# Kernel optimization log

Measured on AMD Instinct MI355X. Metric: run time of the kernel, lower is better.

The kernel has to match this reference:

```python
import jax, jax.numpy as jnp
import numpy as np

EPS = 1e-5
NEG = -1000000.0
H = 8

def layer_norm(v, g, b):
    mu = jnp.mean(v, axis=-1, keepdims=True)
    var = jnp.var(v, axis=-1, keepdims=True)
    return (v - mu) * jax.lax.rsqrt(var + EPS) * g + b

def setup_inputs() -> dict:
    key = jax.random.key(0)
    ks = jax.random.split(key, 12)
    B, T, Tc, D, Dc = 8, 2048, 512, 1024, 512
    s = lambda fan: 1.0 / np.sqrt(fan)
    return {
        'query': jax.random.normal(ks[0], (B, T, D), jnp.float32),
        'x': jax.random.normal(ks[1], (B, T, D), jnp.float32),
        'cond_emb': jax.random.normal(ks[2], (B, Tc, Dc), jnp.float32),
        'src_mask': jax.random.uniform(ks[3], (B, T, 1), jnp.float32),
        'cond_mask': jax.random.uniform(ks[4], (B, Tc, 1), jnp.float32),
        'norm_x_g': jnp.ones((D,), jnp.float32),
        'norm_x_b': jnp.zeros((D,), jnp.float32),
        'norm_c_g': jnp.ones((Dc,), jnp.float32),
        'norm_c_b': jnp.zeros((Dc,), jnp.float32),
        'W_kc': jax.random.normal(ks[5], (D, Dc), jnp.float32) * s(Dc),
        'b_kc': jnp.zeros((D,), jnp.float32),
        'W_vc': jax.random.normal(ks[6], (D, Dc), jnp.float32) * s(Dc),
        'b_vc': jnp.zeros((D,), jnp.float32),
        'W_kx': jax.random.normal(ks[7], (D, D), jnp.float32) * s(D),
        'b_kx': jnp.zeros((D,), jnp.float32),
        'W_vx': jax.random.normal(ks[8], (D, D), jnp.float32) * s(D),
        'b_vx': jnp.zeros((D,), jnp.float32),
        'W_y': jax.random.normal(ks[9], (D, D), jnp.float32) * s(D),
        'b_y': jnp.zeros((D,), jnp.float32),
    }

def reference(query, x, cond_emb, src_mask, cond_mask,
              norm_x_g, norm_x_b, norm_c_g, norm_c_b,
              W_kc, b_kc, W_vc, b_vc, W_kx, b_kx, W_vx, b_vx, W_y, b_y):
    B, T, D = x.shape
    Tc = cond_emb.shape[1]
    N = T + Tc
    xn = layer_norm(x, norm_x_g, norm_x_b)          # (B,T,D)
    cn = layer_norm(cond_emb, norm_c_g, norm_c_b)   # (B,Tc,Dc)
    # keys with additive mask penalty, concatenated over sequence dim
    k_cond = cn @ W_kc.T + b_kc + (1.0 - cond_mask) * NEG
    k_x = xn @ W_kx.T + b_kx + (1.0 - src_mask) * NEG
    key = jnp.concatenate([k_cond, k_x], axis=1)    # (B,N,D)
    q = jax.nn.softmax(query.reshape(B, T, H, D // H), axis=-1)
    k = jax.nn.softmax(key.reshape(B, N, H, D // H), axis=1)
    v_cond = (cn @ W_vc.T + b_vc) * cond_mask
    v_x = (xn @ W_vx.T + b_vx) * src_mask
    v = jnp.concatenate([v_cond, v_x], axis=1).reshape(B, N, H, D // H)
    attn = jnp.einsum('bnhd,bnhl->bhdl', k, v)      # (B,H,d,d) linear-attention KV
    y = jnp.einsum('bthd,bhdl->bthl', q, attn).reshape(B, T, D)
    return y @ W_y.T + b_y
```

## Files before the change

kernel.cpp:

```cpp
#include <hip/hip_runtime.h>


typedef short s16x8 __attribute__((ext_vector_type(8)));
typedef float f32x4 __attribute__((ext_vector_type(4)));

__device__ __forceinline__ float b2f(short s) {
    unsigned int u = ((unsigned int)(unsigned short)s) << 16;
    return __uint_as_float(u);
}
__device__ __forceinline__ short f2b(float f) {
    unsigned int u = __float_as_uint(f);
    u += 0x7fffu + ((u >> 16) & 1u);
    return (short)(u >> 16);
}

typedef void __attribute__((address_space(1)))* gas_ptr;
typedef void __attribute__((address_space(3)))* las_ptr;
__device__ __forceinline__ void async_cp16(const void* g, void* l) {
    __builtin_amdgcn_global_load_lds((gas_ptr)g, (las_ptr)l, 16, 0, 0);
}

__device__ __forceinline__ float pen_of(const float* __restrict__ cmask,
                                        const float* __restrict__ smask,
                                        int b, int n) {
    float mk = (n < 512) ? cmask[b * 512 + n] : smask[b * 2048 + n - 512];
    return (1.0f - mk) * -1000000.0f;
}

__global__ __launch_bounds__(256) void cvt_kernel(const float* __restrict__ in,
                                                  short* __restrict__ out, int n) {
    int i = (blockIdx.x * 256 + threadIdx.x) * 4;
    if (i < n) {
        float4 v = *(const float4*)&in[i];
        short4 o;
        o.x = f2b(v.x); o.y = f2b(v.y); o.z = f2b(v.z); o.w = f2b(v.w);
        *(short4*)&out[i] = o;
    }
}

__global__ __launch_bounds__(256) void ln_kernel(const float* __restrict__ x,
                                                 const float* __restrict__ g,
                                                 const float* __restrict__ be,
                                                 short* __restrict__ out, int L) {
    long row = blockIdx.x;
    const float* xr = x + row * L;
    short* orow = out + row * L;
    int tid = threadIdx.x;
    int i0 = tid * 4;
    bool active = i0 < L;
    float v0 = 0.f, v1 = 0.f, v2 = 0.f, v3 = 0.f;
    if (active) {
        float4 p = *(const float4*)&xr[i0];
        v0 = p.x; v1 = p.y; v2 = p.z; v3 = p.w;
    }
    float s = v0 + v1 + v2 + v3;
    float s2 = v0*v0 + v1*v1 + v2*v2 + v3*v3;
    #pragma unroll
    for (int off = 32; off > 0; off >>= 1) {
        s  += __shfl_down(s, off);
        s2 += __shfl_down(s2, off);
    }
    __shared__ float ss[4], sq[4];
    int wave = tid >> 6, lane = tid & 63;
    if (lane == 0) { ss[wave] = s; sq[wave] = s2; }
    __syncthreads();
    if (tid == 0) {
        float t1 = ss[0] + ss[1] + ss[2] + ss[3];
        float t2 = sq[0] + sq[1] + sq[2] + sq[3];
        float mu = t1 / (float)L;
        float var = t2 / (float)L - mu * mu;
        ss[0] = mu;
        sq[0] = rsqrtf(var + 1e-5f);
    }
    __syncthreads();
    float mu = ss[0], rs = sq[0];
    if (active) {
        float4 gp = *(const float4*)&g[i0];
        float4 bp = *(const float4*)&be[i0];
        short4 o;
        o.x = f2b((v0 - mu) * rs * gp.x + bp.x);
        o.y = f2b((v1 - mu) * rs * gp.y + bp.y);
        o.z = f2b((v2 - mu) * rs * gp.z + bp.z);
        o.w = f2b((v3 - mu) * rs * gp.w + bp.w);
        *(short4*)&orow[i0] = o;
    }
}

__global__ __launch_bounds__(256) void qsoftmax_kernel(const float* __restrict__ q,
                                                       short* __restrict__ out) {
    long row = (long)blockIdx.x * 4 + (threadIdx.x >> 6);
    int lane = threadIdx.x & 63;
    const float* qr = q + row * 128;
    float2 p = *(const float2*)&qr[lane * 2];
    float v0 = p.x, v1 = p.y;
    float m = fmaxf(v0, v1);
    #pragma unroll
    for (int off = 32; off > 0; off >>= 1) m = fmaxf(m, __shfl_xor(m, off));
    float e0 = __expf(v0 - m), e1 = __expf(v1 - m);
    float s = e0 + e1;
    #pragma unroll
    for (int off = 32; off > 0; off >>= 1) s += __shfl_xor(s, off);
    float inv = 1.0f / s;
    short2 o; o.x = f2b(e0 * inv); o.y = f2b(e1 * inv);
    *(short2*)&out[row * 128 + lane * 2] = o;
}

__global__ __launch_bounds__(256) void kstats1(const short* __restrict__ klog,
                                               const float* __restrict__ cmask,
                                               const float* __restrict__ smask,
                                               float* __restrict__ partM,
                                               float* __restrict__ partS) {
    int c = blockIdx.x * 256 + threadIdx.x;
    int b = blockIdx.y;
    int n0 = blockIdx.z * 256;
    const short* base = klog + (long)b * 2560 * 1024 + c;
    float m = -3.4e38f, s = 0.f;
    for (int k = 0; k < 256; ++k) {
        int n = n0 + k;
        float v = b2f(base[(long)n * 1024]) + pen_of(cmask, smask, b, n);
        float nm = fmaxf(m, v);
        s = s * __expf(m - nm) + __expf(v - nm);
        m = nm;
    }
    long o = ((long)(b * 10 + blockIdx.z)) * 1024 + c;
    partM[o] = m;
    partS[o] = s;
}

__global__ __launch_bounds__(256) void kstats2(const float* __restrict__ partM,
                                               const float* __restrict__ partS,
                                               float* __restrict__ Ms,
                                               float* __restrict__ iSs) {
    int c = blockIdx.x * 256 + threadIdx.x;
    int b = blockIdx.y;
    float M = -3.4e38f;
    #pragma unroll
    for (int k = 0; k < 10; ++k)
        M = fmaxf(M, partM[((long)(b * 10 + k)) * 1024 + c]);
    float S = 0.f;
    #pragma unroll
    for (int k = 0; k < 10; ++k) {
        long o = ((long)(b * 10 + k)) * 1024 + c;
        S += partS[o] * __expf(partM[o] - M);
    }
    Ms[b * 1024 + c] = M;
    iSs[b * 1024 + c] = 1.0f / S;
}

template<int MODE>
__global__ __launch_bounds__(256) void gemm_bt(
        const short* __restrict__ A, int lda, long strideA,
        const short* __restrict__ B, int ldb, long strideB,
        void* __restrict__ Out, int ldo, long strideO,
        int K,
        const float* __restrict__ bias,
        const float* __restrict__ mask, long strideMask) {
    __shared__ short As[128 * 64];
    __shared__ short Bs[128 * 64];
    int tid = threadIdx.x;
    int wave = tid >> 6, lane = tid & 63;
    int n0 = blockIdx.x * 128;
    int m0 = blockIdx.y * 128;
    int z = blockIdx.z;

    const short* Ab;
    const short* Bb;
    if (MODE == 2) {
        int b = z >> 3, h = z & 7;
        Ab = A + (long)b * strideA + h * 128;
        Bb = B + (long)z * 128 * 128;
    } else {
        Ab = A + (long)z * strideA;
        Bb = B + (long)z * strideB;
    }

    f32x4 acc[4][4];
    #pragma unroll
    for (int i = 0; i < 4; ++i)
        #pragma unroll
        for (int j = 0; j < 4; ++j) {
            f32x4 zz = {0.f, 0.f, 0.f, 0.f};
            acc[i][j] = zz;
        }

    int wm = wave >> 1, wn = wave & 1;
    int r = lane & 15, q = lane >> 4;

    for (int k0 = 0; k0 < K; k0 += 64) {
        __syncthreads();
        #pragma unroll
        for (int it = 0; it < 4; ++it) {
            int e = (it * 256 + tid) * 8;
            int row = e >> 6, kk = e & 63;
            const short* ga = Ab + (long)(m0 + row) * lda + k0 + kk;
            const short* gb = Bb + (long)(n0 + row) * ldb + k0 + kk;
            async_cp16(ga, &As[e]);
            async_cp16(gb, &Bs[e]);
        }
        __syncthreads();
        #pragma unroll
        for (int kk = 0; kk < 64; kk += 32) {
            s16x8 af[4], bfr[4];
            #pragma unroll
            for (int i = 0; i < 4; ++i) {
                af[i]  = *(const s16x8*)&As[(wm * 64 + i * 16 + r) * 64 + kk + q * 8];
                bfr[i] = *(const s16x8*)&Bs[(wn * 64 + i * 16 + r) * 64 + kk + q * 8];
            }
            #pragma unroll
            for (int i = 0; i < 4; ++i)
                #pragma unroll
                for (int j = 0; j < 4; ++j)
                    acc[i][j] = __builtin_amdgcn_mfma_f32_16x16x32_bf16(af[i], bfr[j], acc[i][j], 0, 0, 0);
        }
    }

    #pragma unroll
    for (int i = 0; i < 4; ++i) {
        int gmb = m0 + wm * 64 + i * 16 + q * 4;
        #pragma unroll
        for (int j = 0; j < 4; ++j) {
            int gn = n0 + wn * 64 + j * 16 + r;
            #pragma unroll
            for (int rg = 0; rg < 4; ++rg) {
                int row = gmb + rg;
                float v = acc[i][j][rg];
                if (MODE == 1) {
                    float bi = bias[gn];
                    float mk = mask[(long)z * strideMask + row];
                    ((short*)Out)[(long)z * strideO + (long)row * ldo + gn] =
                        f2b((v + bi) * mk);
                } else if (MODE == 2) {
                    int b = z >> 3, h = z & 7;
                    ((short*)Out)[(long)b * strideO + (long)row * ldo + h * 128 + gn] = f2b(v);
                } else if (MODE == 3) {
                    float bi = bias[gn];
                    ((short*)Out)[(long)z * strideO + (long)row * ldo + gn] = f2b(v + bi);
                } else {
                    float bi = bias[gn];
                    ((float*)Out)[(long)z * strideO + (long)row * ldo + gn] = v + bi;
                }
            }
        }
    }
}

__global__ __launch_bounds__(256) void attn_part(const short* __restrict__ klog,
                                                 const short* __restrict__ vbuf,
                                                 const float* __restrict__ cmask,
                                                 const float* __restrict__ smask,
                                                 const float* __restrict__ Ms,
                                                 float* __restrict__ pbuf) {
    __shared__ short kT[128 * 64];
    __shared__ short vT[128 * 64];
    int ns = blockIdx.x;
    int z = blockIdx.y;
    int b = z >> 3, h = z & 7;
    int tid = threadIdx.x;
    int wave = tid >> 6, lane = tid & 63;
    int r = lane & 15, q = lane >> 4;
    int wm = wave >> 1, wn = wave & 1;

    int cg = h * 128 + lane * 2;
    float M0 = Ms[b * 1024 + cg];
    float M1 = Ms[b * 1024 + cg + 1];

    f32x4 acc[4][4];
    #pragma unroll
    for (int i = 0; i < 4; ++i)
        #pragma unroll
        for (int j = 0; j < 4; ++j) {
            f32x4 zz = {0.f, 0.f, 0.f, 0.f};
            acc[i][j] = zz;
        }

    long base = ((long)b * 2560) * 1024 + h * 128;
    int nbase = ns * 320;
    int swz = (lane & 7) << 3;
    for (int n0 = 0; n0 < 320; n0 += 64) {
        __syncthreads();
        #pragma unroll 4
        for (int i = 0; i < 16; ++i) {
            int nl = i * 4 + wave;
            int n = nbase + n0 + nl;
            float pen = pen_of(cmask, smask, b, n);
            long g = base + (long)n * 1024 + lane * 2;
            short2 k2 = *(const short2*)&klog[g];
            short2 v2 = *(const short2*)&vbuf[g];
            float w0 = __expf(b2f(k2.x) + pen - M0);
            float w1 = __expf(b2f(k2.y) + pen - M1);
            int c = lane * 2;
            int sw = nl ^ swz;
            kT[c * 64 + sw] = f2b(w0);
            kT[(c + 1) * 64 + sw] = f2b(w1);
            vT[c * 64 + sw] = v2.x;
            vT[(c + 1) * 64 + sw] = v2.y;
        }
        __syncthreads();
        #pragma unroll
        for (int kk = 0; kk < 64; kk += 32) {
            s16x8 af[4], bfr[4];
            #pragma unroll
            for (int i = 0; i < 4; ++i) {
                int cA = wm * 64 + i * 16 + r;
                int cB = wn * 64 + i * 16 + r;
                af[i]  = *(const s16x8*)&kT[cA * 64 + ((kk + q * 8) ^ (((cA >> 1) & 7) << 3))];
                bfr[i] = *(const s16x8*)&vT[cB * 64 + ((kk + q * 8) ^ (((cB >> 1) & 7) << 3))];
            }
            #pragma unroll
            for (int i = 0; i < 4; ++i)
                #pragma unroll
                for (int j = 0; j < 4; ++j)
                    acc[i][j] = __builtin_amdgcn_mfma_f32_16x16x32_bf16(af[i], bfr[j], acc[i][j], 0, 0, 0);
        }
    }
    float* outp = pbuf + ((long)z * 8 + ns) * 16384;
    #pragma unroll
    for (int i = 0; i < 4; ++i) {
        int d0 = wm * 64 + i * 16 + q * 4;
        #pragma unroll
        for (int j = 0; j < 4; ++j) {
            int l = wn * 64 + j * 16 + r;
            *(f32x4*)&outp[l * 128 + d0] = acc[i][j];
        }
    }
}

__global__ __launch_bounds__(256) void reduce_attn(const float* __restrict__ pbuf,
                                                   const float* __restrict__ iSs,
                                                   short* __restrict__ attnT) {
    int idx = blockIdx.x * 256 + threadIdx.x;
    int z = idx >> 14, rem = idx & 16383;
    int d = rem & 127;
    int b = z >> 3, h = z & 7;
    const float* p = pbuf + (long)z * 8 * 16384 + rem;
    float s = 0.f;
    #pragma unroll
    for (int ns = 0; ns < 8; ++ns) s += p[ns * 16384];
    attnT[idx] = f2b(s * iSs[b * 1024 + h * 128 + d]);
}

extern "C" void kernel_launch(void* const* d_in, const int* in_sizes, int n_in,
                              void* d_out, int out_size, void* d_ws, size_t ws_size,
                              hipStream_t stream) {
    const float* query = (const float*)d_in[0];
    const float* x     = (const float*)d_in[1];
    const float* cond  = (const float*)d_in[2];
    const float* smask = (const float*)d_in[3];
    const float* cmask = (const float*)d_in[4];
    const float* gx  = (const float*)d_in[5];
    const float* bx  = (const float*)d_in[6];
    const float* gc  = (const float*)d_in[7];
    const float* bc  = (const float*)d_in[8];
    const float* Wkc = (const float*)d_in[9];
    const float* bkc = (const float*)d_in[10];
    const float* Wvc = (const float*)d_in[11];
    const float* bvc = (const float*)d_in[12];
    const float* Wkx = (const float*)d_in[13];
    const float* bkx = (const float*)d_in[14];
    const float* Wvx = (const float*)d_in[15];
    const float* bvx = (const float*)d_in[16];
    const float* Wy  = (const float*)d_in[17];
    const float* by  = (const float*)d_in[18];

    size_t o_xn    = 0;
    size_t o_cn    = o_xn    + 33554432;
    size_t o_klog  = o_cn    + 4194304;
    size_t o_vbuf  = o_klog  + 41943040;
    size_t o_qsm   = o_vbuf  + 41943040;
    size_t o_attnT = o_qsm   + 33554432;
    size_t o_partM = o_attnT + 2097152;
    size_t o_partS = o_partM + 327680;
    size_t o_Ms    = o_partS + 327680;
    size_t o_iSs   = o_Ms    + 32768;
    size_t o_wkc   = o_iSs   + 32768;
    size_t o_wvc   = o_wkc   + 1048576;
    size_t o_wkx   = o_wvc   + 1048576;
    size_t o_wvx   = o_wkx   + 2097152;
    size_t o_wy    = o_wvx   + 2097152;
    size_t need    = o_wy    + 2097152;
    if (ws_size < need) return;

    char* w = (char*)d_ws;
    short* xn    = (short*)(w + o_xn);
    short* cn    = (short*)(w + o_cn);
    short* klog  = (short*)(w + o_klog);
    short* vbuf  = (short*)(w + o_vbuf);
    short* qsm   = (short*)(w + o_qsm);
    short* attnT = (short*)(w + o_attnT);
    float* partM = (float*)(w + o_partM);
    float* partS = (float*)(w + o_partS);
    float* Ms    = (float*)(w + o_Ms);
    float* iSs   = (float*)(w + o_iSs);
    short* wkc   = (short*)(w + o_wkc);
    short* wvc   = (short*)(w + o_wvc);
    short* wkx   = (short*)(w + o_wkx);
    short* wvx   = (short*)(w + o_wvx);
    short* wy    = (short*)(w + o_wy);
    short* ybuf  = klog;
    float* pbuf  = (float*)xn;

    cvt_kernel<<<512, 256, 0, stream>>>(Wkc, wkc, 524288);
    cvt_kernel<<<512, 256, 0, stream>>>(Wvc, wvc, 524288);
    cvt_kernel<<<1024, 256, 0, stream>>>(Wkx, wkx, 1048576);
    cvt_kernel<<<1024, 256, 0, stream>>>(Wvx, wvx, 1048576);
    cvt_kernel<<<1024, 256, 0, stream>>>(Wy, wy, 1048576);

    ln_kernel<<<16384, 256, 0, stream>>>(x, gx, bx, xn, 1024);
    ln_kernel<<<4096, 256, 0, stream>>>(cond, gc, bc, cn, 512);
    qsoftmax_kernel<<<32768, 256, 0, stream>>>(query, qsm);

    gemm_bt<3><<<dim3(8, 16, 8), 256, 0, stream>>>(
        xn, 1024, 2097152L, wkx, 1024, 0L,
        klog + 512 * 1024, 1024, 2621440L,
        1024, bkx, nullptr, 0L);
    gemm_bt<3><<<dim3(8, 4, 8), 256, 0, stream>>>(
        cn, 512, 262144L, wkc, 512, 0L,
        klog, 1024, 2621440L,
        512, bkc, nullptr, 0L);
    gemm_bt<1><<<dim3(8, 16, 8), 256, 0, stream>>>(
        xn, 1024, 2097152L, wvx, 1024, 0L,
        vbuf + 512 * 1024, 1024, 2621440L,
        1024, bvx, smask, 2048L);
    gemm_bt<1><<<dim3(8, 4, 8), 256, 0, stream>>>(
        cn, 512, 262144L, wvc, 512, 0L,
        vbuf, 1024, 2621440L,
        512, bvc, cmask, 512L);

    kstats1<<<dim3(4, 8, 10), 256, 0, stream>>>(klog, cmask, smask, partM, partS);
    kstats2<<<dim3(4, 8), 256, 0, stream>>>(partM, partS, Ms, iSs);

    attn_part<<<dim3(8, 64), 256, 0, stream>>>(klog, vbuf, cmask, smask, Ms, pbuf);
    reduce_attn<<<4096, 256, 0, stream>>>(pbuf, iSs, attnT);

    gemm_bt<2><<<dim3(1, 16, 64), 256, 0, stream>>>(
        qsm, 1024, 2097152L, attnT, 128, 16384L,
        ybuf, 1024, 2097152L,
        128, nullptr, nullptr, 0L);
    gemm_bt<4><<<dim3(8, 128, 1), 256, 0, stream>>>(
        ybuf, 1024, 0L, wy, 1024, 0L,
        d_out, 1024, 0L,
        1024, by, nullptr, 0L);
}
```

Baseline: 531.2 us.

## Fold output projection into per-batch attention, fuse K/V GEMMs, swizzle LDS

Several changes land together. The five weight conversions become one launch. The K and V projections share a single GEMM over the concatenated [Wk;Wv] weight (N=2048), so the normalized activations are read once. The LDS tiles get an XOR swizzle to avoid bank conflicts. The output projection is reassociated as q·(attn·Wy^T): a small per-batch Z = Wy·attnD is computed first and then one GEMM takes qsm to the output, which replaces the two-step y-then-Wy pipeline and removes the ybuf round trip. This costs a per-batch Z buffer (8 MB bf16) and a changed rounding order.

Result: no change. 528.5 us (-0.5%).

```diff
diff --git a/kernel.cpp b/kernel.cpp
--- a/kernel.cpp
+++ b/kernel.cpp
@@ -27,15 +27,23 @@
     return (1.0f - mk) * -1000000.0f;
 }
 
-__global__ __launch_bounds__(256) void cvt_kernel(const float* __restrict__ in,
-                                                  short* __restrict__ out, int n) {
-    int i = (blockIdx.x * 256 + threadIdx.x) * 4;
-    if (i < n) {
-        float4 v = *(const float4*)&in[i];
-        short4 o;
-        o.x = f2b(v.x); o.y = f2b(v.y); o.z = f2b(v.z); o.w = f2b(v.w);
-        *(short4*)&out[i] = o;
-    }
+__global__ __launch_bounds__(256) void cvt_all(const float* __restrict__ Wkc,
+                                               const float* __restrict__ Wvc,
+                                               const float* __restrict__ Wkx,
+                                               const float* __restrict__ Wvx,
+                                               const float* __restrict__ Wy,
+                                               short* __restrict__ dst) {
+    int g = (blockIdx.x * 256 + threadIdx.x) * 4;
+    const float* src;
+    if (g < 524288)        src = Wkc + g;
+    else if (g < 1048576)  src = Wvc + (g - 524288);
+    else if (g < 2097152)  src = Wkx + (g - 1048576);
+    else if (g < 3145728)  src = Wvx + (g - 2097152);
+    else                   src = Wy  + (g - 3145728);
+    float4 v = *(const float4*)src;
+    short4 o;
+    o.x = f2b(v.x); o.y = f2b(v.y); o.z = f2b(v.z); o.w = f2b(v.w);
+    *(short4*)&dst[g] = o;
 }
 
 __global__ __launch_bounds__(256) void ln_kernel(const float* __restrict__ x,
@@ -150,10 +158,11 @@
 template<int MODE>
 __global__ __launch_bounds__(256) void gemm_bt(
         const short* __restrict__ A, int lda, long strideA,
-        const short* __restrict__ B, int ldb, long strideB,
-        void* __restrict__ Out, int ldo, long strideO,
+        const short* __restrict__ B, int ldb,
+        void* __restrict__ OutA, void* __restrict__ OutB,
+        int ldo, long strideO,
         int K,
-        const float* __restrict__ bias,
+        const float* __restrict__ biasK, const float* __restrict__ biasV,
         const float* __restrict__ mask, long strideMask) {
     __shared__ short As[128 * 64];
     __shared__ short Bs[128 * 64];
@@ -166,12 +175,14 @@
     const short* Ab;
     const short* Bb;
     if (MODE == 2) {
-        int b = z >> 3, h = z & 7;
-        Ab = A + (long)b * strideA + h * 128;
-        Bb = B + (long)z * 128 * 128;
+        Ab = A + (z & 7) * 128;
+        Bb = B + (long)z * 16384;
+    } else if (MODE == 4) {
+        Ab = A + (long)z * strideA;
+        Bb = B + (long)z * 1048576;
     } else {
         Ab = A + (long)z * strideA;
-        Bb = B + (long)z * strideB;
+        Bb = B;
     }
 
     f32x4 acc[4][4];
@@ -190,12 +201,14 @@
         __syncthreads();
         #pragma unroll
         for (int it = 0; it < 4; ++it) {
-            int e = (it * 256 + tid) * 8;
-            int row = e >> 6, kk = e & 63;
-            const short* ga = Ab + (long)(m0 + row) * lda + k0 + kk;
-            const short* gb = Bb + (long)(n0 + row) * ldb + k0 + kk;
-            async_cp16(ga, &As[e]);
-            async_cp16(gb, &Bs[e]);
+            int cid = it * 256 + tid;
+            int row = cid >> 3;
+            int c8  = cid & 7;
+            int col = ((c8 ^ (row & 7)) << 3);
+            const short* ga = Ab + (long)(m0 + row) * lda + k0 + col;
+            const short* gb = Bb + (long)(n0 + row) * ldb + k0 + col;
+            async_cp16(ga, &As[cid * 8]);
+            async_cp16(gb, &Bs[cid * 8]);
         }
         __syncthreads();
         #pragma unroll
@@ -203,8 +216,11 @@
             s16x8 af[4], bfr[4];
             #pragma unroll
             for (int i = 0; i < 4; ++i) {
-                af[i]  = *(const s16x8*)&As[(wm * 64 + i * 16 + r) * 64 + kk + q * 8];
-                bfr[i] = *(const s16x8*)&Bs[(wn * 64 + i * 16 + r) * 64 + kk + q * 8];
+                int rowA = wm * 64 + i * 16 + r;
+                int rowB = wn * 64 + i * 16 + r;
+                int ch = (kk >> 3) + q;
+                af[i]  = *(const s16x8*)&As[rowA * 64 + ((ch ^ (rowA & 7)) << 3)];
+                bfr[i] = *(const s16x8*)&Bs[rowB * 64 + ((ch ^ (rowB & 7)) << 3)];
             }
             #pragma unroll
             for (int i = 0; i < 4; ++i)
@@ -224,20 +240,22 @@
             for (int rg = 0; rg < 4; ++rg) {
                 int row = gmb + rg;
                 float v = acc[i][j][rg];
-                if (MODE == 1) {
-                    float bi = bias[gn];
-                    float mk = mask[(long)z * strideMask + row];
-                    ((short*)Out)[(long)z * strideO + (long)row * ldo + gn] =
-                        f2b((v + bi) * mk);
+                if (MODE == 0) {
+                    if (gn < 1024) {
+                        ((short*)OutA)[(long)z * strideO + (long)row * ldo + gn] =
+                            f2b(v + biasK[gn]);
+                    } else {
+                        int gv = gn - 1024;
+                        float mk = mask[(long)z * strideMask + row];
+                        ((short*)OutB)[(long)z * strideO + (long)row * ldo + gv] =
+                            f2b((v + biasV[gv]) * mk);
+                    }
                 } else if (MODE == 2) {
-                    int b = z >> 3, h = z & 7;
-                    ((short*)Out)[(long)b * strideO + (long)row * ldo + h * 128 + gn] = f2b(v);
-                } else if (MODE == 3) {
-                    float bi = bias[gn];
-                    ((short*)Out)[(long)z * strideO + (long)row * ldo + gn] = f2b(v + bi);
+                    ((short*)OutA)[(long)(z >> 3) * 1048576 + (long)row * 1024 +
+                                   (z & 7) * 128 + gn] = f2b(v);
                 } else {
-                    float bi = bias[gn];
-                    ((float*)Out)[(long)z * strideO + (long)row * ldo + gn] = v + bi;
+                    ((float*)OutA)[(long)z * strideO + (long)row * ldo + gn] =
+                        v + biasK[gn];
                 }
             }
         }
@@ -327,16 +345,16 @@
 
 __global__ __launch_bounds__(256) void reduce_attn(const float* __restrict__ pbuf,
                                                    const float* __restrict__ iSs,
-                                                   short* __restrict__ attnT) {
+                                                   short* __restrict__ attnD) {
     int idx = blockIdx.x * 256 + threadIdx.x;
     int z = idx >> 14, rem = idx & 16383;
-    int d = rem & 127;
+    int d = rem & 127, l = rem >> 7;
     int b = z >> 3, h = z & 7;
     const float* p = pbuf + (long)z * 8 * 16384 + rem;
     float s = 0.f;
     #pragma unroll
     for (int ns = 0; ns < 8; ++ns) s += p[ns * 16384];
-    attnT[idx] = f2b(s * iSs[b * 1024 + h * 128 + d]);
+    attnD[(long)z * 16384 + d * 128 + l] = f2b(s * iSs[b * 1024 + h * 128 + d]);
 }
 
 extern "C" void kernel_launch(void* const* d_in, const int* in_sizes, int n_in,
@@ -367,8 +385,8 @@
     size_t o_klog  = o_cn    + 4194304;
     size_t o_vbuf  = o_klog  + 41943040;
     size_t o_qsm   = o_vbuf  + 41943040;
-    size_t o_attnT = o_qsm   + 33554432;
-    size_t o_partM = o_attnT + 2097152;
+    size_t o_attnD = o_qsm   + 33554432;
+    size_t o_partM = o_attnD + 2097152;
     size_t o_partS = o_partM + 327680;
     size_t o_Ms    = o_partS + 327680;
     size_t o_iSs   = o_Ms    + 32768;
@@ -386,58 +404,44 @@
     short* klog  = (short*)(w + o_klog);
     short* vbuf  = (short*)(w + o_vbuf);
     short* qsm   = (short*)(w + o_qsm);
-    short* attnT = (short*)(w + o_attnT);
+    short* attnD = (short*)(w + o_attnD);
     float* partM = (float*)(w + o_partM);
     float* partS = (float*)(w + o_partS);
     float* Ms    = (float*)(w + o_Ms);
     float* iSs   = (float*)(w + o_iSs);
     short* wkc   = (short*)(w + o_wkc);
-    short* wvc   = (short*)(w + o_wvc);
     short* wkx   = (short*)(w + o_wkx);
-    short* wvx   = (short*)(w + o_wvx);
     short* wy    = (short*)(w + o_wy);
-    short* ybuf  = klog;
     float* pbuf  = (float*)xn;
-
-    cvt_kernel<<<512, 256, 0, stream>>>(Wkc, wkc, 524288);
-    cvt_kernel<<<512, 256, 0, stream>>>(Wvc, wvc, 524288);
-    cvt_kernel<<<1024, 256, 0, stream>>>(Wkx, wkx, 1048576);
-    cvt_kernel<<<1024, 256, 0, stream>>>(Wvx, wvx, 1048576);
-    cvt_kernel<<<1024, 256, 0, stream>>>(Wy, wy, 1048576);
+    short* Zt    = klog;
+
+    cvt_all<<<4096, 256, 0, stream>>>(Wkc, Wvc, Wkx, Wvx, Wy, wkc);
 
     ln_kernel<<<16384, 256, 0, stream>>>(x, gx, bx, xn, 1024);
     ln_kernel<<<4096, 256, 0, stream>>>(cond, gc, bc, cn, 512);
     qsoftmax_kernel<<<32768, 256, 0, stream>>>(query, qsm);
 
-    gemm_bt<3><<<dim3(8, 16, 8), 256, 0, stream>>>(
-        xn, 1024, 2097152L, wkx, 1024, 0L,
-        klog + 512 * 1024, 1024, 2621440L,
-        1024, bkx, nullptr, 0L);
-    gemm_bt<3><<<dim3(8, 4, 8), 256, 0, stream>>>(
-        cn, 512, 262144L, wkc, 512, 0L,
-        klog, 1024, 2621440L,
-        512, bkc, nullptr, 0L);
-    gemm_bt<1><<<dim3(8, 16, 8), 256, 0, stream>>>(
-        xn, 1024, 2097152L, wvx, 1024, 0L,
-        vbuf + 512 * 1024, 1024, 2621440L,
-        1024, bvx, smask, 2048L);
-    gemm_bt<1><<<dim3(8, 4, 8), 256, 0, stream>>>(
-        cn, 512, 262144L, wvc, 512, 0L,
-        vbuf, 1024, 2621440L,
-        512, bvc, cmask, 512L);
+    gemm_bt<0><<<dim3(16, 16, 8), 256, 0, stream>>>(
+        xn, 1024, 2097152L, wkx, 1024,
+        klog + 512 * 1024, vbuf + 512 * 1024, 1024, 2621440L,
+        1024, bkx, bvx, smask, 2048L);
+    gemm_bt<0><<<dim3(16, 4, 8), 256, 0, stream>>>(
+        cn, 512, 262144L, wkc, 512,
+        klog, vbuf, 1024, 2621440L,
+        512, bkc, bvc, cmask, 512L);
 
     kstats1<<<dim3(4, 8, 10), 256, 0, stream>>>(klog, cmask, smask, partM, partS);
     kstats2<<<dim3(4, 8), 256, 0, stream>>>(partM, partS, Ms, iSs);
 
     attn_part<<<dim3(8, 64), 256, 0, stream>>>(klog, vbuf, cmask, smask, Ms, pbuf);
-    reduce_attn<<<4096, 256, 0, stream>>>(pbuf, iSs, attnT);
-
-    gemm_bt<2><<<dim3(1, 16, 64), 256, 0, stream>>>(
-        qsm, 1024, 2097152L, attnT, 128, 16384L,
-        ybuf, 1024, 2097152L,
-        128, nullptr, nullptr, 0L);
-    gemm_bt<4><<<dim3(8, 128, 1), 256, 0, stream>>>(
-        ybuf, 1024, 0L, wy, 1024, 0L,
-        d_out, 1024, 0L,
-        1024, by, nullptr, 0L);
-}
+    reduce_attn<<<4096, 256, 0, stream>>>(pbuf, iSs, attnD);
+
+    gemm_bt<2><<<dim3(1, 8, 64), 256, 0, stream>>>(
+        wy, 1024, 0L, attnD, 128,
+        Zt, nullptr, 1024, 0L,
+        128, nullptr, nullptr, nullptr, 0L);
+    gemm_bt<4><<<dim3(8, 16, 8), 256, 0, stream>>>(
+        qsm, 1024, 2097152L, Zt, 1024,
+        d_out, nullptr, 1024, 2097152L,
+        1024, by, nullptr, nullptr, 0L);
+}
```
